# Kernel tuning notes

Hardware: AMD Instinct MI355X
Metric: run time of the kernel (lower is better)

## Reference

```python
import jax, jax.numpy as jnp
import numpy as np

HAD_BLOCK = 128
HAD_SCALE = 2.0 ** (-3.5)  # 1/sqrt(128), orthonormal block Hadamard


def _hadamard_matrix(n):
    H = np.array([[1.0]], dtype=np.float32)
    while H.shape[0] < n:
        H = np.block([[H, H], [H, -H]])
    return jnp.asarray(H)

_H = _hadamard_matrix(HAD_BLOCK)


def hadamard_transform(x, scale):
    # x: (..., D) with D % 128 == 0; blockwise Hadamard rotation on last dim
    shp = x.shape
    xb = x.reshape(shp[:-1] + (shp[-1] // HAD_BLOCK, HAD_BLOCK))
    y = jnp.einsum('...b,cb->...c', xb, _H) * scale
    return y.reshape(shp)


def setup_inputs() -> dict:
    key = jax.random.key(0)
    kx, kw, kb = jax.random.split(key, 3)
    B, S, IN, OUT = 4, 2048, 4096, 4096
    x = jax.random.normal(kx, (B, S, IN), dtype=jnp.float32)
    # master fp weight, then preprocess: Hadamard-rotate rows, quantize to int4,
    # pack two nibbles per element (per-out-channel scale/add)
    w = jax.random.normal(kw, (OUT, IN), dtype=jnp.float32) / np.float32(np.sqrt(IN))
    w_had = hadamard_transform(w, HAD_SCALE)
    wmin = w_had.min(axis=1, keepdims=True)
    wmax = w_had.max(axis=1, keepdims=True)
    w_scale = jnp.maximum((wmax - wmin) / 15.0, 1e-8)  # [OUT,1]
    w_add = wmin                                        # [OUT,1]
    w_int = jnp.clip(jnp.round((w_had - w_add) / w_scale), 0, 15).astype(jnp.int32)
    w_int_packed = (w_int[:, ::2] | (w_int[:, 1::2] << 4)).astype(jnp.int32)  # [OUT, IN//2]
    bias = jax.random.normal(kb, (OUT,), dtype=jnp.float32) * 0.01
    return {"x": x, "w_int_packed": w_int_packed, "w_scale": w_scale,
            "w_add": w_add, "bias": bias}


def reference(x, w_int_packed, w_scale, w_add, bias):
    OUT = w_int_packed.shape[0]
    IN = w_int_packed.shape[1] * 2
    # unpack int4 nibbles -> [OUT, IN]
    low = w_int_packed & 0xF
    high = (w_int_packed >> 4) & 0xF
    w_int = jnp.stack([low, high], axis=-1).reshape(OUT, IN).astype(w_scale.dtype)
    # per-out-channel dequant
    w_deq = w_int * w_scale + w_add  # [OUT, IN]
    # fused Hadamard rotation on activations (matches rotated weight)
    a = hadamard_transform(x, HAD_SCALE)  # [B,S,IN]
    y = jnp.einsum('bsi,oi->bso', a, w_deq)
    return y + bias
```

## Files before the change

kernel.cpp:

```cpp
#include <hip/hip_runtime.h>
#include <hip/hip_bf16.h>
#include <hip/hip_fp16.h>

#define IN_DIM 4096
#define OUT_DIM 4096
#define HAD_SCALE_F 0.08838834764831845f

typedef int   i32x4 __attribute__((ext_vector_type(4)));
typedef float f32x4 __attribute__((ext_vector_type(4)));

__global__ __launch_bounds__(256)
void had_rows_q(const float* __restrict__ x, short* __restrict__ aq,
                float* __restrict__ rowsum, float* __restrict__ srow)
{
    __shared__ float wmx[4];
    __shared__ int   wqs[4];
    const int tid  = threadIdx.x;
    const int lane = tid & 63;
    const int wv   = tid >> 6;
    const size_t row = blockIdx.x;
    const float* xr = x + row * IN_DIM;

    float2 v[8];
    #pragma unroll
    for (int b = 0; b < 8; ++b) {
        const int blk = wv * 8 + b;
        v[b] = *(const float2*)&xr[blk * 128 + lane * 2];
    }

    float smax = 0.f;
    #pragma unroll
    for (int b = 0; b < 8; ++b) {
        const float a = v[b].x + v[b].y;
        const float d = v[b].x - v[b].y;
        v[b].x = a; v[b].y = d;
        #pragma unroll
        for (int m = 1; m <= 32; m <<= 1) {
            const float px = __shfl_xor(v[b].x, m, 64);
            const float py = __shfl_xor(v[b].y, m, 64);
            const float s  = (lane & m) ? -1.0f : 1.0f;
            v[b].x = fmaf(s, v[b].x, px);
            v[b].y = fmaf(s, v[b].y, py);
        }
        v[b].x *= HAD_SCALE_F;
        v[b].y *= HAD_SCALE_F;
        smax = fmaxf(smax, fmaxf(fabsf(v[b].x), fabsf(v[b].y)));
    }

    #pragma unroll
    for (int off = 32; off > 0; off >>= 1)
        smax = fmaxf(smax, __shfl_xor(smax, off, 64));
    if (lane == 0) wmx[wv] = smax;
    __syncthreads();
    const float mx  = fmaxf(fmaxf(wmx[0], wmx[1]), fmaxf(wmx[2], wmx[3]));
    const float inv = (mx > 0.f) ? 127.0f / mx : 0.f;
    const float sa  = mx * (1.0f / 127.0f);

    int qsum = 0;
    #pragma unroll
    for (int b = 0; b < 8; ++b) {
        const int blk = wv * 8 + b;
        const int q0 = (int)rintf(v[b].x * inv);
        const int q1 = (int)rintf(v[b].y * inv);
        qsum += q0 + q1;
        aq[(row * IN_DIM + blk * 128 + lane * 2) >> 1] =
            (short)((q0 & 0xFF) | ((q1 & 0xFF) << 8));
    }
    #pragma unroll
    for (int off = 32; off > 0; off >>= 1) qsum += __shfl_xor(qsum, off, 64);
    if (lane == 0) wqs[wv] = qsum;
    __syncthreads();
    if (tid == 0) {
        rowsum[row] = sa * (float)((wqs[0] + wqs[1]) + (wqs[2] + wqs[3]));
        srow[row]   = sa;
    }
}

__global__ __launch_bounds__(256)
void unpack_w8(const int* __restrict__ wp, signed char* __restrict__ wf8)
{
    const int gid = blockIdx.x * 256 + threadIdx.x;
    const int n   = gid >> 9;
    const int k0  = (gid & 511) * 8;
    const int4 p  = *(const int4*)(wp + (size_t)n * (IN_DIM / 2) + (k0 >> 1));
    const unsigned lo = (unsigned)(p.x & 15) | ((unsigned)((p.x >> 4) & 15) << 8)
                      | ((unsigned)(p.y & 15) << 16) | ((unsigned)((p.y >> 4) & 15) << 24);
    const unsigned hi = (unsigned)(p.z & 15) | ((unsigned)((p.z >> 4) & 15) << 8)
                      | ((unsigned)(p.w & 15) << 16) | ((unsigned)((p.w >> 4) & 15) << 24);
    *(uint2*)(wf8 + (size_t)n * IN_DIM + k0) = make_uint2(lo, hi);
}

#define NT (IN_DIM / 128)
#define NI (NT / 2)

#define BAR()        asm volatile("s_barrier" ::: "memory")
#define WAIT_VM(N)   asm volatile("s_waitcnt vmcnt(" #N ")" ::: "memory")

#define STAGE_A(p, R, kt) __builtin_amdgcn_global_load_lds( \
    (const __attribute__((address_space(1))) void*)(sA + (((size_t)(R)) << 18) + (((size_t)((kt) & 31)) << 7)), \
    (__attribute__((address_space(3))) void*)(smem + (p) * 65536 + (R) * 8192 + dstA), 16, 0, 0)
#define STAGE_B(p, R, kt) __builtin_amdgcn_global_load_lds( \
    (const __attribute__((address_space(1))) void*)(sB + (((size_t)(R)) << 18) + (((size_t)((kt) & 31)) << 7)), \
    (__attribute__((address_space(3))) void*)(smem + (p) * 65536 + (R) * 8192 + dstB), 16, 0, 0)

#define LDA(p, mq, mi, kb) (*(const i32x4*)(smem + (p)*65536 + (mq)*8192 + (mi)*2048 + aOffK[kb]))
#define LDB(p, nq, ni, kb) (*(const i32x4*)(smem + (p)*65536 + (nq)*4096 + (ni)*2048 + bOffK[kb]))

#define LOAD_A_TO(dst, p, mq) do { \
    _Pragma("unroll") for (int mi = 0; mi < 4; ++mi) { \
        dst[mi][0] = LDA(p, mq, mi, 0); \
        dst[mi][1] = LDA(p, mq, mi, 1); \
    } } while (0)

#define LOAD_B(p, nq) do { \
    _Pragma("unroll") for (int ni = 0; ni < 2; ++ni) { \
        bfr[(nq)*2+ni][0] = LDB(p, nq, ni, 0); \
        bfr[(nq)*2+ni][1] = LDB(p, nq, ni, 1); \
    } } while (0)

#define MFMA_Q(abuf, mq, nq) do { \
    __builtin_amdgcn_s_setprio(1); \
    _Pragma("unroll") for (int mi = 0; mi < 4; ++mi) \
    _Pragma("unroll") for (int ni = 0; ni < 2; ++ni) \
    _Pragma("unroll") for (int kb = 0; kb < 2; ++kb) \
        acc[(mq)*4+mi][(nq)*2+ni] = __builtin_amdgcn_mfma_i32_16x16x64_i8( \
            abuf[mi][kb], bfr[(nq)*2+ni][kb], acc[(mq)*4+mi][(nq)*2+ni], 0, 0, 0); \
    __builtin_amdgcn_s_setprio(0); \
} while (0)

__global__ __launch_bounds__(512, 2)
void gemm_i8(const signed char* __restrict__ Aq, const signed char* __restrict__ Bw,
             const float* __restrict__ wscale, const float* __restrict__ wadd,
             const float* __restrict__ bias, const float* __restrict__ rowsum,
             const float* __restrict__ srow, float* __restrict__ out)
{
    __shared__ char smem[131072];

    const int tid  = threadIdx.x;
    const int lane = tid & 63;
    const int w    = tid >> 6;
    const int wm   = w >> 2;
    const int wn   = w & 3;

    const int bid = blockIdx.x;
    const int wg  = (bid & 7) * 64 + (bid >> 3);
    const int m0  = (wg >> 4) * 256;
    const int n0  = (wg & 15) * 256;

    const int rt = tid >> 3;
    const int ct = (tid & 7) ^ (rt & 7);
    const signed char* sA = Aq + (size_t)(m0 + rt) * IN_DIM + ct * 16;
    const signed char* sB = Bw + (size_t)(n0 + rt) * IN_DIM + ct * 16;
    const int dstA = w * 1024;
    const int dstB = 32768 + w * 1024;

    const int l15 = lane & 15, g = lane >> 4, l7 = lane & 7;
    const int s0 = (g ^ l7) << 4;
    int aOffK[2], bOffK[2];
    aOffK[0] = (wm * 128 + l15) * 128 + s0;
    aOffK[1] = (wm * 128 + l15) * 128 + (s0 ^ 64);
    bOffK[0] = 32768 + (wn * 64 + l15) * 128 + s0;
    bOffK[1] = 32768 + (wn * 64 + l15) * 128 + (s0 ^ 64);

    i32x4 afrA[4][2], afrB[4][2], bfr[4][2];
    i32x4 acc[8][4] = {};

    #pragma unroll
    for (int R = 0; R < 4; ++R) { STAGE_A(0, R, 0); STAGE_B(0, R, 0); }
    #pragma unroll
    for (int R = 0; R < 4; ++R) { STAGE_A(1, R, 1); STAGE_B(1, R, 1); }
    WAIT_VM(8);
    BAR();
    LOAD_B(0, 0);
    LOAD_A_TO(afrA, 0, 0);

    #pragma unroll 1
    for (int it = 0; it < NI; ++it) {
        const int kt1 = 2 * it + 1;
        const int kt2 = (2 * it + 2) & (NT - 1);
        const int kt3 = (2 * it + 3) & (NT - 1);

        LOAD_B(0, 1);
        if (it) { STAGE_B(1, 2, kt1); STAGE_B(1, 3, kt1);
                  STAGE_A(1, 1, kt1); STAGE_A(1, 3, kt1); }
        MFMA_Q(afrA, 0, 0);
        LOAD_A_TO(afrB, 0, 1);
        MFMA_Q(afrA, 0, 1);
        if (it) { WAIT_VM(2); } else { WAIT_VM(0); }
        BAR();

        STAGE_B(0, 0, kt2); STAGE_B(0, 1, kt2);
        MFMA_Q(afrB, 1, 0);
        LOAD_B(1, 0);
        LOAD_A_TO(afrA, 1, 0);
        STAGE_A(0, 0, kt2); STAGE_A(0, 2, kt2);
        MFMA_Q(afrB, 1, 1);
        WAIT_VM(4);
        BAR();

        STAGE_B(0, 2, kt2); STAGE_B(0, 3, kt2);
        MFMA_Q(afrA, 0, 0);
        LOAD_B(1, 1);
        LOAD_A_TO(afrB, 1, 1);
        STAGE_A(0, 1, kt2); STAGE_A(0, 3, kt2);
        MFMA_Q(afrA, 0, 1);
        WAIT_VM(2);
        BAR();

        STAGE_B(1, 0, kt3); STAGE_B(1, 1, kt3);
        MFMA_Q(afrB, 1, 0);
        LOAD_B(0, 0);
        LOAD_A_TO(afrA, 0, 0);
        STAGE_A(1, 0, kt3); STAGE_A(1, 2, kt3);
        MFMA_Q(afrB, 1, 1);
        WAIT_VM(4);
        BAR();
    }

    #pragma unroll
    for (int n = 0; n < 4; ++n) {
        const int col = n0 + wn * 64 + n * 16 + l15;
        const float sc = wscale[col];
        const float ad = wadd[col];
        const float bi = bias[col];
        #pragma unroll
        for (int m = 0; m < 8; ++m) {
            const int row = m0 + wm * 128 + m * 16 + g * 4;
            const float4 rs4 = *(const float4*)&rowsum[row];
            const float4 sr4 = *(const float4*)&srow[row];
            #pragma unroll
            for (int j = 0; j < 4; ++j) {
                const float rs = (j == 0) ? rs4.x : (j == 1) ? rs4.y : (j == 2) ? rs4.z : rs4.w;
                const float sr = (j == 0) ? sr4.x : (j == 1) ? sr4.y : (j == 2) ? sr4.z : sr4.w;
                out[(size_t)(row + j) * OUT_DIM + col] =
                    (float)acc[m][n][j] * (sc * sr) + ad * rs + bi;
            }
        }
    }
}

extern "C" void kernel_launch(void* const* d_in, const int* in_sizes, int n_in,
                              void* d_out, int out_size, void* d_ws, size_t ws_size,
                              hipStream_t stream)
{
    const float* x      = (const float*)d_in[0];
    const int*   wp     = (const int*)d_in[1];
    const float* wscale = (const float*)d_in[2];
    const float* wadd   = (const float*)d_in[3];
    const float* bias   = (const float*)d_in[4];
    float*       out    = (float*)d_out;

    const int M = in_sizes[0] / IN_DIM;

    char* ws = (char*)d_ws;
    signed char* wf8 = (signed char*)ws;
    const size_t wf_bytes = (size_t)OUT_DIM * IN_DIM;
    short* aq = (short*)(ws + wf_bytes);
    const size_t aq_bytes = (size_t)M * IN_DIM;
    float* rowsum = (float*)(ws + wf_bytes + aq_bytes);
    float* srow   = (float*)(ws + wf_bytes + aq_bytes + (size_t)M * 4);

    const int unpack_blocks = (OUT_DIM * (IN_DIM / 8)) / 256;
    unpack_w8<<<unpack_blocks, 256, 0, stream>>>(wp, wf8);

    had_rows_q<<<M, 256, 0, stream>>>(x, aq, rowsum, srow);

    gemm_i8<<<(M / 256) * (OUT_DIM / 256), 512, 0, stream>>>(
        (const signed char*)aq, wf8, wscale, wadd, bias, rowsum, srow, out);
}
```

Baseline: 183.7 us.

## Switch GEMM to 32x32x32 int8 MFMA and vectorize Hadamard quantization

The int8 GEMM replaces 16x16x64 MFMA tiles with 32x32x32 MFMA tiles. It adjusts the LDS fragment addressing, accumulator layout and epilogue row/column mapping to match. The aim is fewer MFMA issues and fewer LDS fragment reads per unit of work. Separately, the Hadamard quant kernel now has each thread do a 16-point in-register butterfly plus 3 shuffle stages, with one 16-byte packed store in place of many 2-byte stores. The risk is higher register pressure from the larger accumulators and possible LDS bank conflicts under the new swizzle.

```diff
diff --git a/kernel.cpp b/kernel.cpp
--- a/kernel.cpp
+++ b/kernel.cpp
@@ -6,69 +6,80 @@
 #define OUT_DIM 4096
 #define HAD_SCALE_F 0.08838834764831845f
 
-typedef int   i32x4 __attribute__((ext_vector_type(4)));
-typedef float f32x4 __attribute__((ext_vector_type(4)));
+typedef int   i32x4  __attribute__((ext_vector_type(4)));
+typedef int   i32x16 __attribute__((ext_vector_type(16)));
+typedef float f32x4  __attribute__((ext_vector_type(4)));
 
 __global__ __launch_bounds__(256)
-void had_rows_q(const float* __restrict__ x, short* __restrict__ aq,
+void had_rows_q(const float* __restrict__ x, int* __restrict__ aq,
                 float* __restrict__ rowsum, float* __restrict__ srow)
 {
     __shared__ float wmx[4];
     __shared__ int   wqs[4];
-    const int tid  = threadIdx.x;
-    const int lane = tid & 63;
-    const int wv   = tid >> 6;
+    const int tid = threadIdx.x;
+    const int wv  = tid >> 6;
     const size_t row = blockIdx.x;
-    const float* xr = x + row * IN_DIM;
-
-    float2 v[8];
-    #pragma unroll
-    for (int b = 0; b < 8; ++b) {
-        const int blk = wv * 8 + b;
-        v[b] = *(const float2*)&xr[blk * 128 + lane * 2];
+    const float* xr = x + row * IN_DIM + tid * 16;
+
+    float e[16];
+    #pragma unroll
+    for (int v = 0; v < 4; ++v) {
+        const float4 f = ((const float4*)xr)[v];
+        e[v*4+0] = f.x; e[v*4+1] = f.y; e[v*4+2] = f.z; e[v*4+3] = f.w;
+    }
+
+    #pragma unroll
+    for (int s = 1; s < 16; s <<= 1) {
+        #pragma unroll
+        for (int i = 0; i < 16; ++i) {
+            if (!(i & s)) {
+                const float u = e[i], w2 = e[i | s];
+                e[i]     = u + w2;
+                e[i | s] = u - w2;
+            }
+        }
+    }
+    #pragma unroll
+    for (int m = 1; m <= 4; m <<= 1) {
+        const float sgn = (tid & m) ? -1.0f : 1.0f;
+        #pragma unroll
+        for (int i = 0; i < 16; ++i) {
+            const float p = __shfl_xor(e[i], m, 64);
+            e[i] = fmaf(sgn, e[i], p);
+        }
     }
 
     float smax = 0.f;
     #pragma unroll
-    for (int b = 0; b < 8; ++b) {
-        const float a = v[b].x + v[b].y;
-        const float d = v[b].x - v[b].y;
-        v[b].x = a; v[b].y = d;
-        #pragma unroll
-        for (int m = 1; m <= 32; m <<= 1) {
-            const float px = __shfl_xor(v[b].x, m, 64);
-            const float py = __shfl_xor(v[b].y, m, 64);
-            const float s  = (lane & m) ? -1.0f : 1.0f;
-            v[b].x = fmaf(s, v[b].x, px);
-            v[b].y = fmaf(s, v[b].y, py);
-        }
-        v[b].x *= HAD_SCALE_F;
-        v[b].y *= HAD_SCALE_F;
-        smax = fmaxf(smax, fmaxf(fabsf(v[b].x), fabsf(v[b].y)));
-    }
-
+    for (int i = 0; i < 16; ++i) {
+        e[i] *= HAD_SCALE_F;
+        smax = fmaxf(smax, fabsf(e[i]));
+    }
     #pragma unroll
     for (int off = 32; off > 0; off >>= 1)
         smax = fmaxf(smax, __shfl_xor(smax, off, 64));
-    if (lane == 0) wmx[wv] = smax;
+    if ((tid & 63) == 0) wmx[wv] = smax;
     __syncthreads();
     const float mx  = fmaxf(fmaxf(wmx[0], wmx[1]), fmaxf(wmx[2], wmx[3]));
     const float inv = (mx > 0.f) ? 127.0f / mx : 0.f;
     const float sa  = mx * (1.0f / 127.0f);
 
     int qsum = 0;
-    #pragma unroll
-    for (int b = 0; b < 8; ++b) {
-        const int blk = wv * 8 + b;
-        const int q0 = (int)rintf(v[b].x * inv);
-        const int q1 = (int)rintf(v[b].y * inv);
-        qsum += q0 + q1;
-        aq[(row * IN_DIM + blk * 128 + lane * 2) >> 1] =
-            (short)((q0 & 0xFF) | ((q1 & 0xFF) << 8));
-    }
+    int pk[4];
+    #pragma unroll
+    for (int g2 = 0; g2 < 4; ++g2) {
+        const int q0 = (int)rintf(e[g2*4+0] * inv);
+        const int q1 = (int)rintf(e[g2*4+1] * inv);
+        const int q2 = (int)rintf(e[g2*4+2] * inv);
+        const int q3 = (int)rintf(e[g2*4+3] * inv);
+        qsum += (q0 + q1) + (q2 + q3);
+        pk[g2] = (q0 & 0xFF) | ((q1 & 0xFF) << 8) | ((q2 & 0xFF) << 16) | (q3 << 24);
+    }
+    *(int4*)&aq[row * (IN_DIM / 4) + tid * 4] = make_int4(pk[0], pk[1], pk[2], pk[3]);
+
     #pragma unroll
     for (int off = 32; off > 0; off >>= 1) qsum += __shfl_xor(qsum, off, 64);
-    if (lane == 0) wqs[wv] = qsum;
+    if ((tid & 63) == 0) wqs[wv] = qsum;
     __syncthreads();
     if (tid == 0) {
         rowsum[row] = sa * (float)((wqs[0] + wqs[1]) + (wqs[2] + wqs[3]));
@@ -103,28 +114,26 @@
     (const __attribute__((address_space(1))) void*)(sB + (((size_t)(R)) << 18) + (((size_t)((kt) & 31)) << 7)), \
     (__attribute__((address_space(3))) void*)(smem + (p) * 65536 + (R) * 8192 + dstB), 16, 0, 0)
 
-#define LDA(p, mq, mi, kb) (*(const i32x4*)(smem + (p)*65536 + (mq)*8192 + (mi)*2048 + aOffK[kb]))
-#define LDB(p, nq, ni, kb) (*(const i32x4*)(smem + (p)*65536 + (nq)*4096 + (ni)*2048 + bOffK[kb]))
+#define LDA(p, Mb, ks) (*(const i32x4*)(smem + (p)*65536 + (Mb)*4096 + (aBase ^ ((ks) << 5))))
+#define LDB(p, Nb, ks) (*(const i32x4*)(smem + (p)*65536 + (Nb)*4096 + (bBase ^ ((ks) << 5))))
 
 #define LOAD_A_TO(dst, p, mq) do { \
-    _Pragma("unroll") for (int mi = 0; mi < 4; ++mi) { \
-        dst[mi][0] = LDA(p, mq, mi, 0); \
-        dst[mi][1] = LDA(p, mq, mi, 1); \
-    } } while (0)
+    _Pragma("unroll") for (int b = 0; b < 2; ++b) \
+    _Pragma("unroll") for (int ks = 0; ks < 4; ++ks) \
+        dst[b][ks] = LDA(p, (mq)*2 + b, ks); \
+    } while (0)
 
 #define LOAD_B(p, nq) do { \
-    _Pragma("unroll") for (int ni = 0; ni < 2; ++ni) { \
-        bfr[(nq)*2+ni][0] = LDB(p, nq, ni, 0); \
-        bfr[(nq)*2+ni][1] = LDB(p, nq, ni, 1); \
-    } } while (0)
+    _Pragma("unroll") for (int ks = 0; ks < 4; ++ks) \
+        bfr[nq][ks] = LDB(p, nq, ks); \
+    } while (0)
 
 #define MFMA_Q(abuf, mq, nq) do { \
     __builtin_amdgcn_s_setprio(1); \
-    _Pragma("unroll") for (int mi = 0; mi < 4; ++mi) \
-    _Pragma("unroll") for (int ni = 0; ni < 2; ++ni) \
-    _Pragma("unroll") for (int kb = 0; kb < 2; ++kb) \
-        acc[(mq)*4+mi][(nq)*2+ni] = __builtin_amdgcn_mfma_i32_16x16x64_i8( \
-            abuf[mi][kb], bfr[(nq)*2+ni][kb], acc[(mq)*4+mi][(nq)*2+ni], 0, 0, 0); \
+    _Pragma("unroll") for (int b = 0; b < 2; ++b) \
+    _Pragma("unroll") for (int ks = 0; ks < 4; ++ks) \
+        acc[(mq)*2+b][nq] = __builtin_amdgcn_mfma_i32_32x32x32_i8( \
+            abuf[b][ks], bfr[nq][ks], acc[(mq)*2+b][nq], 0, 0, 0); \
     __builtin_amdgcn_s_setprio(0); \
 } while (0)
 
@@ -154,16 +163,13 @@
     const int dstA = w * 1024;
     const int dstB = 32768 + w * 1024;
 
-    const int l15 = lane & 15, g = lane >> 4, l7 = lane & 7;
-    const int s0 = (g ^ l7) << 4;
-    int aOffK[2], bOffK[2];
-    aOffK[0] = (wm * 128 + l15) * 128 + s0;
-    aOffK[1] = (wm * 128 + l15) * 128 + (s0 ^ 64);
-    bOffK[0] = 32768 + (wn * 64 + l15) * 128 + s0;
-    bOffK[1] = 32768 + (wn * 64 + l15) * 128 + (s0 ^ 64);
-
-    i32x4 afrA[4][2], afrB[4][2], bfr[4][2];
-    i32x4 acc[8][4] = {};
+    const int r32 = lane & 31, h = lane >> 5;
+    const int sl  = (h ^ (r32 & 7)) << 4;
+    const int aBase = (wm * 128 + r32) * 128 + sl;
+    const int bBase = 32768 + (wn * 64 + r32) * 128 + sl;
+
+    i32x4 afrA[2][4], afrB[2][4], bfr[2][4];
+    i32x16 acc[4][2] = {};
 
     #pragma unroll
     for (int R = 0; R < 4; ++R) { STAGE_A(0, R, 0); STAGE_B(0, R, 0); }
@@ -218,22 +224,25 @@
     }
 
     #pragma unroll
-    for (int n = 0; n < 4; ++n) {
-        const int col = n0 + wn * 64 + n * 16 + l15;
+    for (int Nb = 0; Nb < 2; ++Nb) {
+        const int col = n0 + wn * 64 + Nb * 32 + r32;
         const float sc = wscale[col];
         const float ad = wadd[col];
         const float bi = bias[col];
         #pragma unroll
-        for (int m = 0; m < 8; ++m) {
-            const int row = m0 + wm * 128 + m * 16 + g * 4;
-            const float4 rs4 = *(const float4*)&rowsum[row];
-            const float4 sr4 = *(const float4*)&srow[row];
+        for (int Mb = 0; Mb < 4; ++Mb) {
             #pragma unroll
-            for (int j = 0; j < 4; ++j) {
-                const float rs = (j == 0) ? rs4.x : (j == 1) ? rs4.y : (j == 2) ? rs4.z : rs4.w;
-                const float sr = (j == 0) ? sr4.x : (j == 1) ? sr4.y : (j == 2) ? sr4.z : sr4.w;
-                out[(size_t)(row + j) * OUT_DIM + col] =
-                    (float)acc[m][n][j] * (sc * sr) + ad * rs + bi;
+            for (int q = 0; q < 4; ++q) {
+                const int rbase = m0 + wm * 128 + Mb * 32 + q * 8 + h * 4;
+                const float4 rs4 = *(const float4*)&rowsum[rbase];
+                const float4 sr4 = *(const float4*)&srow[rbase];
+                #pragma unroll
+                for (int j = 0; j < 4; ++j) {
+                    const float rs = (j == 0) ? rs4.x : (j == 1) ? rs4.y : (j == 2) ? rs4.z : rs4.w;
+                    const float sr = (j == 0) ? sr4.x : (j == 1) ? sr4.y : (j == 2) ? sr4.z : sr4.w;
+                    out[(size_t)(rbase + j) * OUT_DIM + col] =
+                        (float)acc[Mb][Nb][q * 4 + j] * (sc * sr) + ad * rs + bi;
+                }
             }
         }
     }
@@ -255,7 +264,7 @@
     char* ws = (char*)d_ws;
     signed char* wf8 = (signed char*)ws;
     const size_t wf_bytes = (size_t)OUT_DIM * IN_DIM;
-    short* aq = (short*)(ws + wf_bytes);
+    int* aq = (int*)(ws + wf_bytes);
     const size_t aq_bytes = (size_t)M * IN_DIM;
     float* rowsum = (float*)(ws + wf_bytes + aq_bytes);
     float* srow   = (float*)(ws + wf_bytes + aq_bytes + (size_t)M * 4);
```

Result: slower. 198.1 us (+7.8%).
